# Optimization experiments

Measured on AMD Instinct MI355X. Metric: run time of the kernel, lower is better.

The kernel has to match this reference:

```python
import jax, jax.numpy as jnp
import numpy as np

BETA_MAX = 0.01
CD_WEIGHT = 1.0
FIDELITY_WEIGHT = 0.5
BETA = BETA_MAX  # fully annealed (step >= beta_warmup)
EPS = 1e-12


def _pairwise_dist(a, b):
    """Euclidean distance matrix. a: [B,N,3], b: [B,M,3] -> [B,N,M]."""
    a2 = jnp.sum(a * a, axis=-1)                      # [B,N]
    b2 = jnp.sum(b * b, axis=-1)                      # [B,M]
    ab = jnp.einsum('bnd,bmd->bnm', a, b)             # [B,N,M]
    sq = a2[:, :, None] + b2[:, None, :] - 2.0 * ab
    return jnp.sqrt(jnp.maximum(sq, EPS))


def chamfer_distance_l1(pred, full):
    d = _pairwise_dist(pred, full)                    # [B,N,M]
    d_pf = jnp.min(d, axis=2)                         # pred -> full, [B,N]
    d_fp = jnp.min(d, axis=1)                         # full -> pred, [B,M]
    return 0.5 * (jnp.mean(d_pf) + jnp.mean(d_fp))


def fidelity_loss(partial, pred):
    # one-directional: every partial point should have a close predicted point
    d = _pairwise_dist(partial, pred)                 # [B,P,N]
    return jnp.mean(jnp.min(d, axis=2))


def kl_divergence(mu, logvar):
    # -0.5 * E_batch[ sum_dim (1 + logvar - mu^2 - exp(logvar)) ]
    kl = -0.5 * jnp.sum(1.0 + logvar - mu * mu - jnp.exp(logvar), axis=1)
    return jnp.mean(kl)


def setup_inputs() -> dict:
    key = jax.random.key(0)
    k1, k2, k3, k4, k5 = jax.random.split(key, 5)
    B, N, P, D = 8, 8192, 2048, 512
    return {
        'pred': jax.random.normal(k1, (B, N, 3), dtype=jnp.float32),
        'full': jax.random.normal(k2, (B, N, 3), dtype=jnp.float32),
        'partial': jax.random.normal(k3, (B, P, 3), dtype=jnp.float32),
        'mu': jax.random.normal(k4, (B, D), dtype=jnp.float32),
        'logvar': jax.random.normal(k5, (B, D), dtype=jnp.float32) * 0.1,
    }


def reference(pred, full, partial, mu, logvar):
    cd = chamfer_distance_l1(pred, full)
    kl = kl_divergence(mu, logvar)
    fidel = fidelity_loss(partial, pred)
    total = CD_WEIGHT * cd + BETA * kl + FIDELITY_WEIGHT * fidel
    return (total, cd, kl, fidel)
```

## Files before the change

kernel.cpp:

```cpp
#include <hip/hip_runtime.h>
#include <math.h>

#define BATCH 8
#define NPTS  8192
#define PPTS  2048
#define DLAT  512

typedef __attribute__((ext_vector_type(8)))  short short8;
typedef __attribute__((ext_vector_type(16))) float floatx16;

#define SEG      (2 * BATCH * NPTS + BATCH * PPTS)
#define DIR_PF   0
#define DIR_FP   (BATCH * NPTS)
#define DIR_FID  (2 * BATCH * NPTS)
#define OFF_SEG  8

#define CHUNK  512
#define XBLK   512

__device__ __forceinline__ unsigned short f2bf(float f) {
    unsigned int u = __float_as_uint(f);
    return (unsigned short)((u + 0x7FFFu + ((u >> 16) & 1u)) >> 16);
}
__device__ __forceinline__ float bf2f(unsigned short s) {
    return __uint_as_float(((unsigned int)s) << 16);
}

__device__ __forceinline__ float min16(floatx16 d, float prev) {
    float a0 = fminf(fminf(d[0],  d[1]),  d[2]);
    float a1 = fminf(fminf(d[3],  d[4]),  d[5]);
    float a2 = fminf(fminf(d[6],  d[7]),  d[8]);
    float a3 = fminf(fminf(d[9],  d[10]), d[11]);
    float a4 = fminf(fminf(d[12], d[13]), d[14]);
    float b0 = fminf(fminf(a0, a1), a2);
    float b1 = fminf(fminf(a3, a4), d[15]);
    return fminf(fminf(b0, b1), prev);
}

__device__ __forceinline__ void encodeY(float y0, float y1, float y2,
                                        uint4* r0, uint4* r1) {
    const unsigned short h0 = f2bf(y0), h1 = f2bf(y1), h2 = f2bf(y2);
    const unsigned short l0 = f2bf(y0 - bf2f(h0));
    const unsigned short l1 = f2bf(y1 - bf2f(h1));
    const unsigned short l2 = f2bf(y2 - bf2f(h2));
    const float yn = fmaf(y0, y0, fmaf(y1, y1, y2 * y2));
    const unsigned short nh = f2bf(yn);
    const unsigned short nl = f2bf(yn - bf2f(nh));
    r0->x = (unsigned int)h0 | ((unsigned int)h1 << 16);
    r0->y = (unsigned int)h2 | ((unsigned int)l0 << 16);
    r0->z = (unsigned int)l1 | ((unsigned int)l2 << 16);
    r0->w = (unsigned int)h0 | ((unsigned int)h1 << 16);
    r1->x = (unsigned int)h2 | ((unsigned int)nh << 16);
    r1->y = (unsigned int)nl;
    r1->z = 0u; r1->w = 0u;
}

__global__ __launch_bounds__(256, 4) void minpass_kernel(
        const float* __restrict__ pred,
        const float* __restrict__ full,
        const float* __restrict__ partial,
        float* __restrict__ wsf,
        int ysplit) {
    const int bid = blockIdx.x;
    const int ys  = bid % ysplit;
    const int r   = bid / ysplit;
    const int b   = r / 36;
    const int s   = r % 36;
    const int yhalf = NPTS / ysplit;

    const int t = threadIdx.x;

    if (bid == 0) {
        if (t < 4) wsf[t] = 0.0f;
        if (t == 4) ((unsigned int*)wsf)[4] = 0u;
    }

    const float* xset; const float* yset; int minoff; int xbase;
    if (s < 16)      { xset = pred;    yset = full; xbase = b*NPTS + s*XBLK;
                       minoff = OFF_SEG + ys*SEG + DIR_PF  + b*NPTS + s*XBLK; }
    else if (s < 32) { xset = full;    yset = pred; xbase = b*NPTS + (s-16)*XBLK;
                       minoff = OFF_SEG + ys*SEG + DIR_FP  + b*NPTS + (s-16)*XBLK; }
    else             { xset = partial; yset = pred; xbase = b*PPTS + (s-32)*XBLK;
                       minoff = OFF_SEG + ys*SEG + DIR_FID + b*PPTS + (s-32)*XBLK; }

    const int lane = t & 63;
    const int wid  = t >> 6;
    const int l31  = lane & 31;
    const int half = lane >> 5;

    __shared__ uint4 sY[2][CHUNK];
    __shared__ uint4 sX[2][XBLK];
    __shared__ float sXn[XBLK];

    for (int i = t; i < XBLK; i += 256) {
        const float* xp = xset + (size_t)(xbase + i) * 3;
        const float x0 = xp[0], x1 = xp[1], x2 = xp[2];
        const float m0 = -2.0f*x0, m1 = -2.0f*x1, m2 = -2.0f*x2;
        const unsigned short h0 = f2bf(m0), h1 = f2bf(m1), h2 = f2bf(m2);
        const unsigned short l0 = f2bf(m0 - bf2f(h0));
        const unsigned short l1 = f2bf(m1 - bf2f(h1));
        const unsigned short l2 = f2bf(m2 - bf2f(h2));
        const unsigned int one = 0x3F80u;
        uint4 r0, r1;
        r0.x = (unsigned int)h0 | ((unsigned int)h1 << 16);
        r0.y = (unsigned int)h2 | ((unsigned int)h0 << 16);
        r0.z = (unsigned int)h1 | ((unsigned int)h2 << 16);
        r0.w = (unsigned int)l0 | ((unsigned int)l1 << 16);
        r1.x = (unsigned int)l2 | (one << 16);
        r1.y = one;
        r1.z = 0u; r1.w = 0u;
        sX[0][i] = r0; sX[1][i] = r1;
        sXn[i] = fmaf(x0, x0, fmaf(x1, x1, x2 * x2));
    }
    __syncthreads();

    const int xw = wid * 128;
    const short8 bf0 = *(const short8*)&sX[half][xw + l31];
    const short8 bf1 = *(const short8*)&sX[half][xw + 32 + l31];
    const short8 bf2 = *(const short8*)&sX[half][xw + 64 + l31];
    const short8 bf3 = *(const short8*)&sX[half][xw + 96 + l31];
    const float  xn0 = sXn[xw + l31];
    const float  xn1 = sXn[xw + 32 + l31];
    const float  xn2 = sXn[xw + 64 + l31];
    const float  xn3 = sXn[xw + 96 + l31];

    const floatx16 zc = {0,0,0,0, 0,0,0,0, 0,0,0,0, 0,0,0,0};
    float cmin0 = 3.4e38f, cmin1 = 3.4e38f, cmin2 = 3.4e38f, cmin3 = 3.4e38f;

    const float* ypts = yset + (size_t)(b * NPTS + ys * yhalf) * 3;

    for (int c = 0; c < yhalf; c += CHUNK) {
        __syncthreads();
        for (int i = t; i < CHUNK; i += 256) {
            const float* yp = ypts + (size_t)(c + i) * 3;
            uint4 r0, r1;
            encodeY(yp[0], yp[1], yp[2], &r0, &r1);
            sY[0][i] = r0; sY[1][i] = r1;
        }
        __syncthreads();

        const uint4* sYh = &sY[half][0];
        short8 af = *(const short8*)&sYh[l31];
#pragma unroll
        for (int j = 0; j < CHUNK / 32; ++j) {
            short8 afn = af;
            if (j + 1 < CHUNK / 32)
                afn = *(const short8*)&sYh[(j + 1) * 32 + l31];
            const floatx16 d0 = __builtin_amdgcn_mfma_f32_32x32x16_bf16(af, bf0, zc, 0, 0, 0);
            const floatx16 d1 = __builtin_amdgcn_mfma_f32_32x32x16_bf16(af, bf1, zc, 0, 0, 0);
            cmin0 = min16(d0, cmin0);
            const floatx16 d2 = __builtin_amdgcn_mfma_f32_32x32x16_bf16(af, bf2, zc, 0, 0, 0);
            cmin1 = min16(d1, cmin1);
            const floatx16 d3 = __builtin_amdgcn_mfma_f32_32x32x16_bf16(af, bf3, zc, 0, 0, 0);
            cmin2 = min16(d2, cmin2);
            cmin3 = min16(d3, cmin3);
            af = afn;
        }
    }

    const float m0 = fminf(cmin0, __shfl_xor(cmin0, 32, 64));
    const float m1 = fminf(cmin1, __shfl_xor(cmin1, 32, 64));
    const float m2 = fminf(cmin2, __shfl_xor(cmin2, 32, 64));
    const float m3 = fminf(cmin3, __shfl_xor(cmin3, 32, 64));
    if (lane < 32) {
        wsf[minoff + xw + l31]      = fmaxf(m0 + xn0, 0.0f);
        wsf[minoff + xw + 32 + l31] = fmaxf(m1 + xn1, 0.0f);
        wsf[minoff + xw + 64 + l31] = fmaxf(m2 + xn2, 0.0f);
        wsf[minoff + xw + 96 + l31] = fmaxf(m3 + xn3, 0.0f);
    }
}

__device__ __forceinline__ float waveReduceSum(float v) {
#pragma unroll
    for (int o = 32; o > 0; o >>= 1) v += __shfl_down(v, o, 64);
    return v;
}

__device__ __forceinline__ float blockReduceSum(float v) {
    __shared__ float wsum[4];
    const int lane = threadIdx.x & 63;
    const int wid  = threadIdx.x >> 6;
    v = waveReduceSum(v);
    if (lane == 0) wsum[wid] = v;
    __syncthreads();
    if (wid == 0) {
        v = (lane < ((int)blockDim.x >> 6)) ? wsum[lane] : 0.0f;
        v = waveReduceSum(v);
    }
    return v;
}

#define NRED_BLOCKS 145
__global__ __launch_bounds__(256) void reduce_finalize_kernel(
        float* __restrict__ wsf,
        const float* __restrict__ mu,
        const float* __restrict__ logvar,
        float* __restrict__ out,
        int ysplit) {
    float* acc = wsf;
    unsigned int* cnt = (unsigned int*)wsf + 4;
    const int bid = blockIdx.x;
    const int t   = threadIdx.x;

    float v = 0.0f;
    int accIdx;
    if (bid < 144) {
        int base;
        if (bid < 64)       { accIdx = 0; base = DIR_PF  + bid * 1024;         }
        else if (bid < 128) { accIdx = 1; base = DIR_FP  + (bid - 64) * 1024;  }
        else                { accIdx = 2; base = DIR_FID + (bid - 128) * 1024; }
#pragma unroll
        for (int k = 0; k < 4; ++k) {
            const int i = OFF_SEG + base + k * 256 + t;
            float m = wsf[i];
            for (int sg = 1; sg < ysplit; ++sg) m = fminf(m, wsf[sg * SEG + i]);
            v += sqrtf(fmaxf(m, 1e-12f));
        }
    } else {
        accIdx = 3;
#pragma unroll
        for (int k = 0; k < BATCH * DLAT / 256; ++k) {
            const int i = k * 256 + t;
            const float m = mu[i];
            const float l = logvar[i];
            v += -0.5f * (1.0f + l - m * m - expf(l));
        }
    }

    v = blockReduceSum(v);
    if (t == 0) {
        atomicAdd(&acc[accIdx], v);
        __threadfence();
        const unsigned int done = atomicAdd(cnt, 1u);
        if (done == NRED_BLOCKS - 1) {
            const float s_pf  = atomicAdd(&acc[0], 0.0f);
            const float s_fp  = atomicAdd(&acc[1], 0.0f);
            const float s_fid = atomicAdd(&acc[2], 0.0f);
            const float s_kl  = atomicAdd(&acc[3], 0.0f);
            const float cd  = 0.5f * (s_pf / (float)(BATCH * NPTS) +
                                      s_fp / (float)(BATCH * NPTS));
            const float fid = s_fid / (float)(BATCH * PPTS);
            const float kl  = s_kl / (float)BATCH;
            out[0] = cd + 0.01f * kl + 0.5f * fid;
            out[1] = cd;
            out[2] = kl;
            out[3] = fid;
        }
    }
}

extern "C" void kernel_launch(void* const* d_in, const int* in_sizes, int n_in,
                              void* d_out, int out_size, void* d_ws, size_t ws_size,
                              hipStream_t stream) {
    const float* pred    = (const float*)d_in[0];
    const float* full    = (const float*)d_in[1];
    const float* partial = (const float*)d_in[2];
    const float* mu      = (const float*)d_in[3];
    const float* logvar  = (const float*)d_in[4];
    float* out = (float*)d_out;
    float* wsf = (float*)d_ws;

    const size_t need4 = (size_t)(OFF_SEG + 4 * SEG) * 4;
    const int ysplit = (ws_size >= need4) ? 4 : 2;

    minpass_kernel<<<8 * 36 * ysplit, 256, 0, stream>>>(pred, full, partial, wsf, ysplit);

    reduce_finalize_kernel<<<NRED_BLOCKS, 256, 0, stream>>>(wsf, mu, logvar, out, ysplit);
}
```

Before: 104.7 us.

## Split Y range eightfold and merge partial minima with atomicMin

Result: no change. 103.6 us, median of 2 (-1.0%).

```diff
diff --git a/kernel.cpp b/kernel.cpp
--- a/kernel.cpp
+++ b/kernel.cpp
@@ -5,6 +5,10 @@
 #define NPTS  8192
 #define PPTS  2048
 #define DLAT  512
+
+#define YSPLIT 8
+#define CHUNK  (NPTS / YSPLIT)
+#define XBLK   512
 
 typedef __attribute__((ext_vector_type(8)))  short short8;
 typedef __attribute__((ext_vector_type(16))) float floatx16;
@@ -14,9 +18,6 @@
 #define DIR_FP   (BATCH * NPTS)
 #define DIR_FID  (2 * BATCH * NPTS)
 #define OFF_SEG  8
-
-#define CHUNK  512
-#define XBLK   512
 
 __device__ __forceinline__ unsigned short f2bf(float f) {
     unsigned int u = __float_as_uint(f);
@@ -59,14 +60,12 @@
         const float* __restrict__ pred,
         const float* __restrict__ full,
         const float* __restrict__ partial,
-        float* __restrict__ wsf,
-        int ysplit) {
+        float* __restrict__ wsf) {
     const int bid = blockIdx.x;
-    const int ys  = bid % ysplit;
-    const int r   = bid / ysplit;
+    const int ys  = bid % YSPLIT;
+    const int r   = bid / YSPLIT;
     const int b   = r / 36;
     const int s   = r % 36;
-    const int yhalf = NPTS / ysplit;
 
     const int t = threadIdx.x;
 
@@ -77,11 +76,11 @@
 
     const float* xset; const float* yset; int minoff; int xbase;
     if (s < 16)      { xset = pred;    yset = full; xbase = b*NPTS + s*XBLK;
-                       minoff = OFF_SEG + ys*SEG + DIR_PF  + b*NPTS + s*XBLK; }
+                       minoff = OFF_SEG + DIR_PF  + b*NPTS + s*XBLK; }
     else if (s < 32) { xset = full;    yset = pred; xbase = b*NPTS + (s-16)*XBLK;
-                       minoff = OFF_SEG + ys*SEG + DIR_FP  + b*NPTS + (s-16)*XBLK; }
+                       minoff = OFF_SEG + DIR_FP  + b*NPTS + (s-16)*XBLK; }
     else             { xset = partial; yset = pred; xbase = b*PPTS + (s-32)*XBLK;
-                       minoff = OFF_SEG + ys*SEG + DIR_FID + b*PPTS + (s-32)*XBLK; }
+                       minoff = OFF_SEG + DIR_FID + b*PPTS + (s-32)*XBLK; }
 
     const int lane = t & 63;
     const int wid  = t >> 6;
@@ -89,11 +88,13 @@
     const int half = lane >> 5;
 
     __shared__ uint4 sY[2][CHUNK];
-    __shared__ uint4 sX[2][XBLK];
-    __shared__ float sXn[XBLK];
-
-    for (int i = t; i < XBLK; i += 256) {
-        const float* xp = xset + (size_t)(xbase + i) * 3;
+
+    const int xw = wid * 128;
+    short8 bf0, bf1, bf2, bf3;
+    float  xn0, xn1, xn2, xn3;
+#pragma unroll
+    for (int k = 0; k < 4; ++k) {
+        const float* xp = xset + (size_t)(xbase + xw + k * 32 + l31) * 3;
         const float x0 = xp[0], x1 = xp[1], x2 = xp[2];
         const float m0 = -2.0f*x0, m1 = -2.0f*x1, m2 = -2.0f*x2;
         const unsigned short h0 = f2bf(m0), h1 = f2bf(m1), h2 = f2bf(m2);
@@ -109,64 +110,65 @@
         r1.x = (unsigned int)l2 | (one << 16);
         r1.y = one;
         r1.z = 0u; r1.w = 0u;
-        sX[0][i] = r0; sX[1][i] = r1;
-        sXn[i] = fmaf(x0, x0, fmaf(x1, x1, x2 * x2));
+        const uint4 rec = half ? r1 : r0;
+        const short8 bfv = *(const short8*)&rec;
+        const float  xnv = fmaf(x0, x0, fmaf(x1, x1, x2 * x2));
+        if (k == 0) { bf0 = bfv; xn0 = xnv; }
+        else if (k == 1) { bf1 = bfv; xn1 = xnv; }
+        else if (k == 2) { bf2 = bfv; xn2 = xnv; }
+        else { bf3 = bfv; xn3 = xnv; }
+    }
+
+    const float* ypts = yset + (size_t)(b * NPTS + ys * CHUNK) * 3;
+    for (int i = t; i < CHUNK; i += 256) {
+        const float* yp = ypts + (size_t)i * 3;
+        uint4 r0, r1;
+        encodeY(yp[0], yp[1], yp[2], &r0, &r1);
+        sY[0][i] = r0; sY[1][i] = r1;
     }
     __syncthreads();
-
-    const int xw = wid * 128;
-    const short8 bf0 = *(const short8*)&sX[half][xw + l31];
-    const short8 bf1 = *(const short8*)&sX[half][xw + 32 + l31];
-    const short8 bf2 = *(const short8*)&sX[half][xw + 64 + l31];
-    const short8 bf3 = *(const short8*)&sX[half][xw + 96 + l31];
-    const float  xn0 = sXn[xw + l31];
-    const float  xn1 = sXn[xw + 32 + l31];
-    const float  xn2 = sXn[xw + 64 + l31];
-    const float  xn3 = sXn[xw + 96 + l31];
 
     const floatx16 zc = {0,0,0,0, 0,0,0,0, 0,0,0,0, 0,0,0,0};
     float cmin0 = 3.4e38f, cmin1 = 3.4e38f, cmin2 = 3.4e38f, cmin3 = 3.4e38f;
 
-    const float* ypts = yset + (size_t)(b * NPTS + ys * yhalf) * 3;
-
-    for (int c = 0; c < yhalf; c += CHUNK) {
-        __syncthreads();
-        for (int i = t; i < CHUNK; i += 256) {
-            const float* yp = ypts + (size_t)(c + i) * 3;
-            uint4 r0, r1;
-            encodeY(yp[0], yp[1], yp[2], &r0, &r1);
-            sY[0][i] = r0; sY[1][i] = r1;
-        }
-        __syncthreads();
-
-        const uint4* sYh = &sY[half][0];
-        short8 af = *(const short8*)&sYh[l31];
-#pragma unroll
-        for (int j = 0; j < CHUNK / 32; ++j) {
-            short8 afn = af;
-            if (j + 1 < CHUNK / 32)
-                afn = *(const short8*)&sYh[(j + 1) * 32 + l31];
-            const floatx16 d0 = __builtin_amdgcn_mfma_f32_32x32x16_bf16(af, bf0, zc, 0, 0, 0);
-            const floatx16 d1 = __builtin_amdgcn_mfma_f32_32x32x16_bf16(af, bf1, zc, 0, 0, 0);
-            cmin0 = min16(d0, cmin0);
-            const floatx16 d2 = __builtin_amdgcn_mfma_f32_32x32x16_bf16(af, bf2, zc, 0, 0, 0);
-            cmin1 = min16(d1, cmin1);
-            const floatx16 d3 = __builtin_amdgcn_mfma_f32_32x32x16_bf16(af, bf3, zc, 0, 0, 0);
-            cmin2 = min16(d2, cmin2);
-            cmin3 = min16(d3, cmin3);
-            af = afn;
-        }
-    }
+    const uint4* sYh = &sY[half][0];
+
+#define JBODY()                                                                         \
+    do {                                                                                \
+        const floatx16 d0 = __builtin_amdgcn_mfma_f32_32x32x16_bf16(af, bf0, zc, 0, 0, 0); \
+        const floatx16 d1 = __builtin_amdgcn_mfma_f32_32x32x16_bf16(af, bf1, zc, 0, 0, 0); \
+        cmin0 = min16(d0, cmin0);                                                       \
+        const floatx16 d2 = __builtin_amdgcn_mfma_f32_32x32x16_bf16(af, bf2, zc, 0, 0, 0); \
+        cmin1 = min16(d1, cmin1);                                                       \
+        const floatx16 d3 = __builtin_amdgcn_mfma_f32_32x32x16_bf16(af, bf3, zc, 0, 0, 0); \
+        cmin2 = min16(d2, cmin2);                                                       \
+        cmin3 = min16(d3, cmin3);                                                       \
+    } while (0)
+
+    short8 af = *(const short8*)&sYh[l31];
+#pragma unroll 8
+    for (int j = 0; j < CHUNK / 32 - 1; ++j) {
+        const short8 afn = *(const short8*)&sYh[(j + 1) * 32 + l31];
+        JBODY();
+        af = afn;
+    }
+    JBODY();
+#undef JBODY
 
     const float m0 = fminf(cmin0, __shfl_xor(cmin0, 32, 64));
     const float m1 = fminf(cmin1, __shfl_xor(cmin1, 32, 64));
     const float m2 = fminf(cmin2, __shfl_xor(cmin2, 32, 64));
     const float m3 = fminf(cmin3, __shfl_xor(cmin3, 32, 64));
     if (lane < 32) {
-        wsf[minoff + xw + l31]      = fmaxf(m0 + xn0, 0.0f);
-        wsf[minoff + xw + 32 + l31] = fmaxf(m1 + xn1, 0.0f);
-        wsf[minoff + xw + 64 + l31] = fmaxf(m2 + xn2, 0.0f);
-        wsf[minoff + xw + 96 + l31] = fmaxf(m3 + xn3, 0.0f);
+        unsigned int* seg = (unsigned int*)wsf;
+        atomicMin(&seg[minoff + xw + l31],
+                  __float_as_uint(fmaxf(m0 + xn0, 0.0f)));
+        atomicMin(&seg[minoff + xw + 32 + l31],
+                  __float_as_uint(fmaxf(m1 + xn1, 0.0f)));
+        atomicMin(&seg[minoff + xw + 64 + l31],
+                  __float_as_uint(fmaxf(m2 + xn2, 0.0f)));
+        atomicMin(&seg[minoff + xw + 96 + l31],
+                  __float_as_uint(fmaxf(m3 + xn3, 0.0f)));
     }
 }
 
@@ -195,8 +197,7 @@
         float* __restrict__ wsf,
         const float* __restrict__ mu,
         const float* __restrict__ logvar,
-        float* __restrict__ out,
-        int ysplit) {
+        float* __restrict__ out) {
     float* acc = wsf;
     unsigned int* cnt = (unsigned int*)wsf + 4;
     const int bid = blockIdx.x;
@@ -212,9 +213,7 @@
 #pragma unroll
         for (int k = 0; k < 4; ++k) {
             const int i = OFF_SEG + base + k * 256 + t;
-            float m = wsf[i];
-            for (int sg = 1; sg < ysplit; ++sg) m = fminf(m, wsf[sg * SEG + i]);
-            v += sqrtf(fmaxf(m, 1e-12f));
+            v += sqrtf(fmaxf(wsf[i], 1e-12f));
         }
     } else {
         accIdx = 3;
@@ -260,10 +259,10 @@
     float* out = (float*)d_out;
     float* wsf = (float*)d_ws;
 
-    const size_t need4 = (size_t)(OFF_SEG + 4 * SEG) * 4;
-    const int ysplit = (ws_size >= need4) ? 4 : 2;
-
-    minpass_kernel<<<8 * 36 * ysplit, 256, 0, stream>>>(pred, full, partial, wsf, ysplit);
-
-    reduce_finalize_kernel<<<NRED_BLOCKS, 256, 0, stream>>>(wsf, mu, logvar, out, ysplit);
-}
+    hipMemsetAsync((char*)d_ws + (size_t)OFF_SEG * sizeof(float), 0x7F,
+                   (size_t)SEG * sizeof(float), stream);
+
+    minpass_kernel<<<8 * 36 * YSPLIT, 256, 0, stream>>>(pred, full, partial, wsf);
+
+    reduce_finalize_kernel<<<NRED_BLOCKS, 256, 0, stream>>>(wsf, mu, logvar, out);
+}
```
